# Optimization experiments

Measured on AMD Instinct MI355X. Metric: run time of the kernel, lower is better.

Reference implementation:

```python
import jax, jax.numpy as jnp
import numpy as np

N_SRC0, N_DST0 = 500000, 65536
N_DST1 = 8192
E0, E1 = 1048576, 131072
H = 4
SLOPE = 0.2


def gat_conv(h_src, h_dst, src, dst, Ws, Wd, al, ar, b, n_dst, act):
    # h_src: [Ns, Fin], Ws: [Fin, H*D]
    D = Ws.shape[1] // H
    fs = (h_src @ Ws).reshape(-1, H, D)          # [Ns,H,D]
    fd = (h_dst @ Wd).reshape(-1, H, D)          # [Nd,H,D]
    el = jnp.einsum('nhd,hd->nh', fs, al)        # [Ns,H]
    er = jnp.einsum('nhd,hd->nh', fd, ar)        # [Nd,H]
    e = jax.nn.leaky_relu(el[src] + er[dst], SLOPE)   # [E,H]
    m = jax.ops.segment_max(e, dst, num_segments=n_dst, indices_are_sorted=True)
    a = jnp.exp(e - m[dst])                      # [E,H]
    s = jax.ops.segment_sum(a, dst, num_segments=n_dst, indices_are_sorted=True)
    alpha = a / s[dst]                           # [E,H]
    msg = fs[src] * alpha[..., None]             # [E,H,D]
    out = jax.ops.segment_sum(msg, dst, num_segments=n_dst, indices_are_sorted=True) + b
    return act(out)                              # [Nd,H,D]


def setup_inputs() -> dict:
    key = jax.random.key(0)
    ks = jax.random.split(key, 16)
    D0, D1 = 64, 47
    inp = {
        'x': jax.random.normal(ks[0], (N_SRC0, 128), jnp.float32),
        'src0': jax.random.randint(ks[1], (E0,), 0, N_SRC0, jnp.int32),
        'dst0': jnp.sort(jax.random.randint(ks[2], (E0,), 0, N_DST0, jnp.int32)),
        'src1': jax.random.randint(ks[3], (E1,), 0, N_DST0, jnp.int32),
        'dst1': jnp.sort(jax.random.randint(ks[4], (E1,), 0, N_DST1, jnp.int32)),
        'Ws0': jax.random.normal(ks[5], (128, H * D0), jnp.float32) * 0.05,
        'Wd0': jax.random.normal(ks[6], (128, H * D0), jnp.float32) * 0.05,
        'al0': jax.random.normal(ks[7], (H, D0), jnp.float32) * 0.05,
        'ar0': jax.random.normal(ks[8], (H, D0), jnp.float32) * 0.05,
        'b0': jax.random.normal(ks[9], (H, D0), jnp.float32) * 0.05,
        'Ws1': jax.random.normal(ks[10], (H * D0, H * D1), jnp.float32) * 0.05,
        'Wd1': jax.random.normal(ks[11], (H * D0, H * D1), jnp.float32) * 0.05,
        'al1': jax.random.normal(ks[12], (H, D1), jnp.float32) * 0.05,
        'ar1': jax.random.normal(ks[13], (H, D1), jnp.float32) * 0.05,
        'b1': jax.random.normal(ks[14], (H, D1), jnp.float32) * 0.05,
    }
    return inp


def reference(x, src0, dst0, src1, dst1, Ws0, Wd0, al0, ar0, b0, Ws1, Wd1, al1, ar1, b1):
    # Layer 0: bipartite GATConv with ReLU, flatten heads
    h_dst = x[:N_DST0]
    h = gat_conv(x, h_dst, src0, dst0, Ws0, Wd0, al0, ar0, b0, N_DST0, jax.nn.relu)
    h = h.reshape(N_DST0, -1)                    # [N_DST0, H*D0]
    # Layer 1: no activation, mean over heads, log_softmax
    h_dst = h[:N_DST1]
    h = gat_conv(h, h_dst, src1, dst1, Ws1, Wd1, al1, ar1, b1, N_DST1, lambda z: z)
    h = h.mean(axis=1)                           # [N_DST1, D1]
    return jax.nn.log_softmax(h, axis=-1)
```

## Files before the change

kernel.cpp:

```cpp
#include <hip/hip_runtime.h>

typedef _Float16 half8  __attribute__((ext_vector_type(8)));
typedef _Float16 half4v __attribute__((ext_vector_type(4)));
typedef float    f32x4  __attribute__((ext_vector_type(4)));

#define GAT_SLOPE 0.2f
#define N_SRC0 500000
#define N_DST0 65536
#define N_DST1 8192
#define E0 1048576
#define E1 131072
#define H 4

__device__ __forceinline__ float leaky(float x) { return x >= 0.f ? x : GAT_SLOPE * x; }

__global__ void collapse_kernel(const float* __restrict__ W, const float* __restrict__ a,
                                float* __restrict__ out, int K, int D) {
  int i = blockIdx.x * 256 + threadIdx.x;
  if (i >= K * 4) return;
  int k = i >> 2, h = i & 3;
  int N = 4 * D;
  float s = 0.f;
  for (int d = 0; d < D; ++d) s += W[(size_t)k * N + h * D + d] * a[h * D + d];
  out[i] = s;
}

__global__ void transposeW_kernel(const float* __restrict__ W, _Float16* __restrict__ WT,
                                  int K, int N) {
  int i = blockIdx.x * 256 + threadIdx.x;
  if (i >= N * K) return;
  int nrow = i / K, k = i - nrow * K;
  WT[i] = (_Float16)W[(size_t)k * N + nrow];
}

__global__ void wstack_kernel(const float* __restrict__ W, _Float16* __restrict__ BTs) {
  int i = blockIdx.x * 256 + threadIdx.x;
  int n = i >> 10, kk = i & 1023;
  int h = kk >> 8, k = kk & 255;
  BTs[i] = (n < 47) ? (_Float16)(0.25f * W[(size_t)k * 188 + h * 47 + n]) : (_Float16)0.f;
}

__global__ void wlr_stack_kernel(const float* __restrict__ wl, const float* __restrict__ wr,
                                 _Float16* __restrict__ out, int K) {
  int i = blockIdx.x * 256 + threadIdx.x;
  if (i >= 16 * K) return;
  int n = i / K, k = i - n * K;
  float v = 0.f;
  if (n < 4) v = wl[k * 4 + n];
  else if (n < 8) v = wr[k * 4 + n - 4];
  out[i] = (_Float16)v;
}

__global__ void seg_starts_kernel(const int* __restrict__ dst, int E, int nseg,
                                  int* __restrict__ seg) {
  int i = blockIdx.x * 256 + threadIdx.x;
  if (i > E) return;
  int lo = (i == 0) ? 0 : dst[i - 1] + 1;
  int hi = (i == E) ? nseg : dst[i];
  for (int d = lo; d <= hi; ++d) seg[d] = i;
}

__global__ __launch_bounds__(256) void score_kernel(
    const int* __restrict__ src, const int* __restrict__ dst,
    const float* __restrict__ el, const float* __restrict__ er,
    float* __restrict__ alpha, int E) {
  int e = blockIdx.x * 256 + threadIdx.x;
  if (e >= E) return;
  int s = src[e], d = dst[e];
  float4 e4 = *(const float4*)(el + (size_t)s * 4);
  float4 r4 = *(const float4*)(er + (size_t)d * 4);
  float4 o;
  o.x = __expf(leaky(e4.x + r4.x));
  o.y = __expf(leaky(e4.y + r4.y));
  o.z = __expf(leaky(e4.z + r4.z));
  o.w = __expf(leaky(e4.w + r4.w));
  *(float4*)(alpha + (size_t)e * 4) = o;
}

__global__ __launch_bounds__(256) void cvt_elr_mfma_kernel(
    const float* __restrict__ x, const _Float16* __restrict__ WLR,
    _Float16* __restrict__ xh, float* __restrict__ el, float* __restrict__ er,
    int M, int n_dst) {
  __shared__ _Float16 As[128 * 128];
  const int t = threadIdx.x, lane = t & 63, wid = t >> 6;
  const int m0 = blockIdx.x * 128;
  for (int i = 0; i < 8; ++i) {
    int c = t + 256 * i;
    int row = c >> 4, j = c & 15;
    int gr = m0 + row;
    half8 va = {};
    if (gr < M) {
      float4 f0 = *(const float4*)(x + (size_t)gr * 128 + j * 8);
      float4 f1 = *(const float4*)(x + (size_t)gr * 128 + j * 8 + 4);
      va[0] = (_Float16)f0.x; va[1] = (_Float16)f0.y;
      va[2] = (_Float16)f0.z; va[3] = (_Float16)f0.w;
      va[4] = (_Float16)f1.x; va[5] = (_Float16)f1.y;
      va[6] = (_Float16)f1.z; va[7] = (_Float16)f1.w;
      *(half8*)(xh + (size_t)gr * 128 + j * 8) = va;
    }
    *(half8*)(&As[row * 128 + ((j ^ (row & 7)) << 3)]) = va;
  }
  half8 bf[4];
  for (int kc = 0; kc < 4; ++kc)
    bf[kc] = *(const half8*)(WLR + (lane & 15) * 128 + kc * 32 + (lane >> 4) * 8);
  __syncthreads();
  f32x4 acc[2] = {};
  for (int rt = 0; rt < 2; ++rt) {
    int row = (wid * 2 + rt) * 16 + (lane & 15);
    for (int kc = 0; kc < 4; ++kc) {
      int chunk = kc * 4 + (lane >> 4);
      half8 af = *(const half8*)(&As[row * 128 + ((chunk ^ (row & 7)) << 3)]);
      acc[rt] = __builtin_amdgcn_mfma_f32_16x16x32_f16(af, bf[kc], acc[rt], 0, 0, 0);
    }
  }
  int col = lane & 15, quad = lane >> 4;
  for (int rt = 0; rt < 2; ++rt)
    for (int r = 0; r < 4; ++r) {
      int row = m0 + (wid * 2 + rt) * 16 + quad * 4 + r;
      if (row < M) {
        if (col < 4) el[(size_t)row * 4 + col] = acc[rt][r];
        else if (col < 8 && row < n_dst) er[(size_t)row * 4 + col - 4] = acc[rt][r];
      }
    }
}

__global__ __launch_bounds__(256) void agg0w_kernel(
    const int* __restrict__ src, const int* __restrict__ seg,
    const float* __restrict__ alpha, const _Float16* __restrict__ xh,
    _Float16* __restrict__ axh) {
  const int lane = threadIdx.x & 63, w = threadIdx.x >> 6;
  const int n = blockIdx.x * 4 + w;
  int s0 = seg[n], s1 = seg[n + 1], len = s1 - s0;
  float a0 = 0.f, a1 = 0.f, a2 = 0.f, a3 = 0.f;
  float t0 = 0.f, t1 = 0.f, t2 = 0.f, t3 = 0.f;
  if (lane < len) {
    float4 v = *(const float4*)(alpha + (size_t)(s0 + lane) * 4);
    a0 = v.x; a1 = v.y; a2 = v.z; a3 = v.w;
    t0 = v.x; t1 = v.y; t2 = v.z; t3 = v.w;
  }
  for (int idx = 64 + lane; idx < len; idx += 64) {
    float4 v = *(const float4*)(alpha + (size_t)(s0 + idx) * 4);
    t0 += v.x; t1 += v.y; t2 += v.z; t3 += v.w;
  }
#pragma unroll
  for (int off = 32; off; off >>= 1) {
    t0 += __shfl_xor(t0, off); t1 += __shfl_xor(t1, off);
    t2 += __shfl_xor(t2, off); t3 += __shfl_xor(t3, off);
  }
  float sinv[4];
  sinv[0] = t0 > 0.f ? 1.f / t0 : 0.f;
  sinv[1] = t1 > 0.f ? 1.f / t1 : 0.f;
  sinv[2] = t2 > 0.f ? 1.f / t2 : 0.f;
  sinv[3] = t3 > 0.f ? 1.f / t3 : 0.f;
  const int g = lane >> 5, ci = lane & 31;
  float A[4][4] = {};
  int iters = (len + 1) >> 1;
  for (int k = 0; k < iters; ++k) {
    int idx = g + 2 * k;
    int sl = idx < 64 ? idx : 0;
    float ah0 = __shfl(a0, sl), ah1 = __shfl(a1, sl);
    float ah2 = __shfl(a2, sl), ah3 = __shfl(a3, sl);
    if (idx >= 64 && idx < len) {
      float4 v = *(const float4*)(alpha + (size_t)(s0 + idx) * 4);
      ah0 = v.x; ah1 = v.y; ah2 = v.z; ah3 = v.w;
    }
    if (idx < len) {
      int sidx = src[s0 + idx];
      half4v xv = *(const half4v*)(xh + (size_t)sidx * 128 + ci * 4);
#pragma unroll
      for (int c = 0; c < 4; ++c) {
        float xc = (float)xv[c];
        A[0][c] += ah0 * xc; A[1][c] += ah1 * xc;
        A[2][c] += ah2 * xc; A[3][c] += ah3 * xc;
      }
    }
  }
#pragma unroll
  for (int h = 0; h < 4; ++h)
#pragma unroll
    for (int c = 0; c < 4; ++c) A[h][c] += __shfl_xor(A[h][c], 32);
  if (g == 0) {
#pragma unroll
    for (int h = 0; h < 4; ++h) {
      half4v o;
#pragma unroll
      for (int c = 0; c < 4; ++c) o[c] = (_Float16)(A[h][c] * sinv[h]);
      *(half4v*)(axh + ((size_t)n * 4 + h) * 128 + ci * 4) = o;
    }
  }
}

__global__ __launch_bounds__(256) void agg1w_kernel(
    const int* __restrict__ src, const int* __restrict__ seg,
    const float* __restrict__ alpha, const _Float16* __restrict__ h0,
    _Float16* __restrict__ axh1) {
  const int lane = threadIdx.x & 63, w = threadIdx.x >> 6;
  const int n = blockIdx.x * 4 + w;
  int s0 = seg[n], s1 = seg[n + 1], len = s1 - s0;
  float a0 = 0.f, a1 = 0.f, a2 = 0.f, a3 = 0.f;
  float t0 = 0.f, t1 = 0.f, t2 = 0.f, t3 = 0.f;
  if (lane < len) {
    float4 v = *(const float4*)(alpha + (size_t)(s0 + lane) * 4);
    a0 = v.x; a1 = v.y; a2 = v.z; a3 = v.w;
    t0 = v.x; t1 = v.y; t2 = v.z; t3 = v.w;
  }
  for (int idx = 64 + lane; idx < len; idx += 64) {
    float4 v = *(const float4*)(alpha + (size_t)(s0 + idx) * 4);
    t0 += v.x; t1 += v.y; t2 += v.z; t3 += v.w;
  }
#pragma unroll
  for (int off = 32; off; off >>= 1) {
    t0 += __shfl_xor(t0, off); t1 += __shfl_xor(t1, off);
    t2 += __shfl_xor(t2, off); t3 += __shfl_xor(t3, off);
  }
  float sinv[4];
  sinv[0] = t0 > 0.f ? 1.f / t0 : 0.f;
  sinv[1] = t1 > 0.f ? 1.f / t1 : 0.f;
  sinv[2] = t2 > 0.f ? 1.f / t2 : 0.f;
  sinv[3] = t3 > 0.f ? 1.f / t3 : 0.f;
  const int g = lane >> 5, ci = lane & 31;
  float A[4][8] = {};
  int iters = (len + 1) >> 1;
  for (int k = 0; k < iters; ++k) {
    int idx = g + 2 * k;
    int sl = idx < 64 ? idx : 0;
    float ah0 = __shfl(a0, sl), ah1 = __shfl(a1, sl);
    float ah2 = __shfl(a2, sl), ah3 = __shfl(a3, sl);
    if (idx >= 64 && idx < len) {
      float4 v = *(const float4*)(alpha + (size_t)(s0 + idx) * 4);
      ah0 = v.x; ah1 = v.y; ah2 = v.z; ah3 = v.w;
    }
    if (idx < len) {
      int sidx = src[s0 + idx];
      half8 xv = *(const half8*)(h0 + (size_t)sidx * 256 + ci * 8);
#pragma unroll
      for (int c = 0; c < 8; ++c) {
        float xc = (float)xv[c];
        A[0][c] += ah0 * xc; A[1][c] += ah1 * xc;
        A[2][c] += ah2 * xc; A[3][c] += ah3 * xc;
      }
    }
  }
#pragma unroll
  for (int h = 0; h < 4; ++h)
#pragma unroll
    for (int c = 0; c < 8; ++c) A[h][c] += __shfl_xor(A[h][c], 32);
  if (g == 0) {
#pragma unroll
    for (int h = 0; h < 4; ++h) {
      half8 o;
#pragma unroll
      for (int c = 0; c < 8; ++c) o[c] = (_Float16)(A[h][c] * sinv[h]);
      *(half8*)(axh1 + ((size_t)n * 4 + h) * 256 + ci * 8) = o;
    }
  }
}

__global__ __launch_bounds__(256) void gemm_h0_kernel(
    const _Float16* __restrict__ axh, const _Float16* __restrict__ BT,
    const float* __restrict__ b, const float* __restrict__ wl1,
    const float* __restrict__ wr1, _Float16* __restrict__ h0,
    float* __restrict__ el1, float* __restrict__ er1) {
  __shared__ _Float16 As[128 * 128];
  __shared__ _Float16 Bs[64 * 128];
  const int t = threadIdx.x, lane = t & 63, wid = t >> 6;
  const int m0 = blockIdx.x * 128;
  const int cl = lane & 15, quad = lane >> 4;
  const int wm = wid * 32;
  f32x4 el1p[2][4] = {}, er1p[2][4] = {};
  for (int h = 0; h < 4; ++h) {
    for (int i = 0; i < 8; ++i) {
      int c = t + 256 * i, row = c >> 4, j = c & 15;
      int sw = ((j ^ (row & 7)) << 3);
      *(half8*)(&As[row * 128 + sw]) =
          *(const half8*)(axh + ((size_t)(m0 + row) * 4 + h) * 128 + j * 8);
    }
    for (int i = 0; i < 4; ++i) {
      int c = t + 256 * i, row = c >> 4, j = c & 15;
      int sw = ((j ^ (row & 7)) << 3);
      *(half8*)(&Bs[row * 128 + sw]) =
          *(const half8*)(BT + (size_t)(h * 64 + row) * 128 + j * 8);
    }
    __syncthreads();
    f32x4 acc[2][4] = {};
    for (int ks = 0; ks < 4; ++ks) {
      int kc = ks * 4 + quad;
      half8 af[2], bf[4];
      for (int i = 0; i < 2; ++i) {
        int ra = wm + 16 * i + cl;
        af[i] = *(const half8*)(&As[ra * 128 + ((kc ^ (ra & 7)) << 3)]);
      }
      for (int j2 = 0; j2 < 4; ++j2) {
        int rb = 16 * j2 + cl;
        bf[j2] = *(const half8*)(&Bs[rb * 128 + ((kc ^ (rb & 7)) << 3)]);
      }
      for (int i = 0; i < 2; ++i)
        for (int j2 = 0; j2 < 4; ++j2)
          acc[i][j2] = __builtin_amdgcn_mfma_f32_16x16x32_f16(af[i], bf[j2], acc[i][j2], 0, 0, 0);
    }
    __syncthreads();
    for (int j2 = 0; j2 < 4; ++j2) {
      int gcol = h * 64 + 16 * j2 + cl;
      float bias = b[gcol];
      f32x4 wlv = *(const f32x4*)(wl1 + (size_t)gcol * 4);
      f32x4 wrv = *(const f32x4*)(wr1 + (size_t)gcol * 4);
      for (int i = 0; i < 2; ++i) {
        int r0 = m0 + wm + 16 * i + quad * 4;
        for (int r = 0; r < 4; ++r) {
          float v = fmaxf(acc[i][j2][r] + bias, 0.f);
          h0[(size_t)(r0 + r) * 256 + gcol] = (_Float16)v;
          el1p[i][r] += wlv * v;
          er1p[i][r] += wrv * v;
        }
      }
    }
  }
#pragma unroll
  for (int off = 1; off < 16; off <<= 1)
#pragma unroll
    for (int i = 0; i < 2; ++i)
#pragma unroll
      for (int r = 0; r < 4; ++r)
#pragma unroll
        for (int c = 0; c < 4; ++c) {
          el1p[i][r][c] += __shfl_xor(el1p[i][r][c], off);
          er1p[i][r][c] += __shfl_xor(er1p[i][r][c], off);
        }
  if (cl == 0) {
    for (int i = 0; i < 2; ++i)
      for (int r = 0; r < 4; ++r) {
        int row = m0 + wm + 16 * i + quad * 4 + r;
        *(f32x4*)(el1 + (size_t)row * 4) = el1p[i][r];
        if (row < N_DST1) *(f32x4*)(er1 + (size_t)row * 4) = er1p[i][r];
      }
  }
}

__global__ __launch_bounds__(256) void gemm_out_kernel(
    const _Float16* __restrict__ axh1, const _Float16* __restrict__ BTs,
    const float* __restrict__ b1, float* __restrict__ out) {
  __shared__ _Float16 As[64 * 128];
  __shared__ _Float16 Bs[64 * 128];
  const int t = threadIdx.x, lane = t & 63, wid = t >> 6;
  const int m0 = blockIdx.x * 64;
  f32x4 acc[4] = {};
  for (int k0 = 0; k0 < 1024; k0 += 128) {
    for (int i = 0; i < 4; ++i) {
      int c = t + 256 * i, row = c >> 4, j = c & 15;
      int sw = ((j ^ (row & 7)) << 3);
      *(half8*)(&As[row * 128 + sw]) =
          *(const half8*)(axh1 + (size_t)(m0 + row) * 1024 + k0 + j * 8);
      *(half8*)(&Bs[row * 128 + sw]) =
          *(const half8*)(BTs + (size_t)row * 1024 + k0 + j * 8);
    }
    __syncthreads();
    const int wm = wid * 16;
    for (int ks = 0; ks < 4; ++ks) {
      int kc = ks * 4 + (lane >> 4);
      int ra = wm + (lane & 15);
      half8 af = *(const half8*)(&As[ra * 128 + ((kc ^ (ra & 7)) << 3)]);
      for (int j2 = 0; j2 < 4; ++j2) {
        int rb = 16 * j2 + (lane & 15);
        half8 bf = *(const half8*)(&Bs[rb * 128 + ((kc ^ (rb & 7)) << 3)]);
        acc[j2] = __builtin_amdgcn_mfma_f32_16x16x32_f16(af, bf, acc[j2], 0, 0, 0);
      }
    }
    __syncthreads();
  }
  int quad = lane >> 4, cl = lane & 15;
  float bm[3];
  for (int j2 = 0; j2 < 3; ++j2) {
    int col = 16 * j2 + cl;
    bm[j2] = (col < 47) ? 0.25f * (b1[col] + b1[col + 47] + b1[col + 94] + b1[col + 141]) : 0.f;
  }
  for (int r = 0; r < 4; ++r) {
    int row = m0 + wid * 16 + quad * 4 + r;
    float v[3];
    float mx = -1e30f;
    for (int j2 = 0; j2 < 3; ++j2) {
      int col = 16 * j2 + cl;
      v[j2] = acc[j2][r] + bm[j2];
      if (col < 47) mx = fmaxf(mx, v[j2]);
    }
    for (int off = 8; off; off >>= 1) mx = fmaxf(mx, __shfl_xor(mx, off));
    float s = 0.f;
    for (int j2 = 0; j2 < 3; ++j2) {
      int col = 16 * j2 + cl;
      if (col < 47) s += __expf(v[j2] - mx);
    }
    for (int off = 8; off; off >>= 1) s += __shfl_xor(s, off);
    float lse = mx + __logf(s);
    for (int j2 = 0; j2 < 3; ++j2) {
      int col = 16 * j2 + cl;
      if (col < 47) out[(size_t)row * 47 + col] = v[j2] - lse;
    }
  }
}

extern "C" void kernel_launch(void* const* d_in, const int* in_sizes, int n_in,
                              void* d_out, int out_size, void* d_ws, size_t ws_size,
                              hipStream_t stream) {
  const float* x   = (const float*)d_in[0];
  const int* src0  = (const int*)d_in[1];
  const int* dst0  = (const int*)d_in[2];
  const int* src1  = (const int*)d_in[3];
  const int* dst1  = (const int*)d_in[4];
  const float* Ws0 = (const float*)d_in[5];
  const float* Wd0 = (const float*)d_in[6];
  const float* al0 = (const float*)d_in[7];
  const float* ar0 = (const float*)d_in[8];
  const float* b0  = (const float*)d_in[9];
  const float* Ws1 = (const float*)d_in[10];
  const float* Wd1 = (const float*)d_in[11];
  const float* al1 = (const float*)d_in[12];
  const float* ar1 = (const float*)d_in[13];
  const float* b1  = (const float*)d_in[14];

  char* w = (char*)d_ws;
  auto alloc = [&](size_t bytes) {
    char* p = w;
    w += (bytes + 255) & ~(size_t)255;
    return p;
  };
  _Float16* xh   = (_Float16*)alloc((size_t)N_SRC0 * 128 * 2);
  _Float16* axh  = (_Float16*)alloc((size_t)N_DST0 * 512 * 2);
  _Float16* h0   = (_Float16*)alloc((size_t)N_DST0 * 256 * 2);
  _Float16* axh1 = (_Float16*)alloc((size_t)N_DST1 * 1024 * 2);
  float* el0     = (float*)alloc((size_t)N_SRC0 * 4 * 4);
  float* er0     = (float*)alloc((size_t)N_DST0 * 4 * 4);
  float* el1     = (float*)alloc((size_t)N_DST0 * 4 * 4);
  float* er1     = (float*)alloc((size_t)N_DST1 * 4 * 4);
  float* alpha0  = (float*)alloc((size_t)E0 * 4 * 4);
  float* alpha1  = (float*)alloc((size_t)E1 * 4 * 4);
  int* seg0      = (int*)alloc((size_t)(N_DST0 + 1) * 4);
  int* seg1      = (int*)alloc((size_t)(N_DST1 + 1) * 4);
  _Float16* BT0  = (_Float16*)alloc(256 * 128 * 2);
  _Float16* BTs  = (_Float16*)alloc(64 * 1024 * 2);
  _Float16* WLR0 = (_Float16*)alloc(16 * 128 * 2);
  float* wl0     = (float*)alloc(128 * 4 * 4);
  float* wr0     = (float*)alloc(128 * 4 * 4);
  float* wl1     = (float*)alloc(256 * 4 * 4);
  float* wr1     = (float*)alloc(256 * 4 * 4);

  collapse_kernel<<<2, 256, 0, stream>>>(Ws0, al0, wl0, 128, 64);
  collapse_kernel<<<2, 256, 0, stream>>>(Wd0, ar0, wr0, 128, 64);
  collapse_kernel<<<4, 256, 0, stream>>>(Ws1, al1, wl1, 256, 47);
  collapse_kernel<<<4, 256, 0, stream>>>(Wd1, ar1, wr1, 256, 47);
  wlr_stack_kernel<<<8, 256, 0, stream>>>(wl0, wr0, WLR0, 128);
  transposeW_kernel<<<128, 256, 0, stream>>>(Ws0, BT0, 128, 256);
  wstack_kernel<<<256, 256, 0, stream>>>(Ws1, BTs);
  seg_starts_kernel<<<(E0 + 1 + 255) / 256, 256, 0, stream>>>(dst0, E0, N_DST0, seg0);
  seg_starts_kernel<<<(E1 + 1 + 255) / 256, 256, 0, stream>>>(dst1, E1, N_DST1, seg1);
  cvt_elr_mfma_kernel<<<(N_SRC0 + 127) / 128, 256, 0, stream>>>(x, WLR0, xh, el0, er0,
                                                                N_SRC0, N_DST0);
  score_kernel<<<E0 / 256, 256, 0, stream>>>(src0, dst0, el0, er0, alpha0, E0);
  agg0w_kernel<<<N_DST0 / 4, 256, 0, stream>>>(src0, seg0, alpha0, xh, axh);
  gemm_h0_kernel<<<N_DST0 / 128, 256, 0, stream>>>(axh, BT0, b0, wl1, wr1, h0, el1, er1);
  score_kernel<<<E1 / 256, 256, 0, stream>>>(src1, dst1, el1, er1, alpha1, E1);
  agg1w_kernel<<<N_DST1 / 4, 256, 0, stream>>>(src1, seg1, alpha1, h0, axh1);
  gemm_out_kernel<<<N_DST1 / 64, 256, 0, stream>>>(axh1, BTs, b1, (float*)d_out);
}
```

Measured before the change: 641.7 us.

## Fuse edge scoring into aggregation kernels and merge prep kernels into one launch

Drops the separate score kernels that wrote per-edge exp scores to global memory. The aggregation kernels now compute leaky-relu and exp on the fly from el[src] and er[dst], and reuse the src index through a lane shuffle. The nine small setup kernels (weight collapse, transposes, segment starts) become one prep kernel. This removes the alpha buffers' write and read traffic and several launches, at the cost of extra exp work and el gathers inside the aggregation kernels.

Result: faster. 544.3 us (-15.2%).

```diff
diff --git a/kernel.cpp b/kernel.cpp
--- a/kernel.cpp
+++ b/kernel.cpp
@@ -14,68 +14,71 @@
 
 __device__ __forceinline__ float leaky(float x) { return x >= 0.f ? x : GAT_SLOPE * x; }
 
-__global__ void collapse_kernel(const float* __restrict__ W, const float* __restrict__ a,
-                                float* __restrict__ out, int K, int D) {
+__global__ __launch_bounds__(256) void prep_kernel(
+    const float* __restrict__ Ws0, const float* __restrict__ Wd0,
+    const float* __restrict__ al0, const float* __restrict__ ar0,
+    const float* __restrict__ Ws1, const float* __restrict__ Wd1,
+    const float* __restrict__ al1, const float* __restrict__ ar1,
+    const int* __restrict__ dst0, const int* __restrict__ dst1,
+    _Float16* __restrict__ BTs, _Float16* __restrict__ BT0,
+    _Float16* __restrict__ WLR0, float* __restrict__ wl1, float* __restrict__ wr1,
+    int* __restrict__ seg0, int* __restrict__ seg1) {
   int i = blockIdx.x * 256 + threadIdx.x;
-  if (i >= K * 4) return;
-  int k = i >> 2, h = i & 3;
-  int N = 4 * D;
-  float s = 0.f;
-  for (int d = 0; d < D; ++d) s += W[(size_t)k * N + h * D + d] * a[h * D + d];
-  out[i] = s;
-}
-
-__global__ void transposeW_kernel(const float* __restrict__ W, _Float16* __restrict__ WT,
-                                  int K, int N) {
-  int i = blockIdx.x * 256 + threadIdx.x;
-  if (i >= N * K) return;
-  int nrow = i / K, k = i - nrow * K;
-  WT[i] = (_Float16)W[(size_t)k * N + nrow];
-}
-
-__global__ void wstack_kernel(const float* __restrict__ W, _Float16* __restrict__ BTs) {
-  int i = blockIdx.x * 256 + threadIdx.x;
-  int n = i >> 10, kk = i & 1023;
-  int h = kk >> 8, k = kk & 255;
-  BTs[i] = (n < 47) ? (_Float16)(0.25f * W[(size_t)k * 188 + h * 47 + n]) : (_Float16)0.f;
-}
-
-__global__ void wlr_stack_kernel(const float* __restrict__ wl, const float* __restrict__ wr,
-                                 _Float16* __restrict__ out, int K) {
-  int i = blockIdx.x * 256 + threadIdx.x;
-  if (i >= 16 * K) return;
-  int n = i / K, k = i - n * K;
-  float v = 0.f;
-  if (n < 4) v = wl[k * 4 + n];
-  else if (n < 8) v = wr[k * 4 + n - 4];
-  out[i] = (_Float16)v;
-}
-
-__global__ void seg_starts_kernel(const int* __restrict__ dst, int E, int nseg,
-                                  int* __restrict__ seg) {
-  int i = blockIdx.x * 256 + threadIdx.x;
-  if (i > E) return;
-  int lo = (i == 0) ? 0 : dst[i - 1] + 1;
-  int hi = (i == E) ? nseg : dst[i];
-  for (int d = lo; d <= hi; ++d) seg[d] = i;
-}
-
-__global__ __launch_bounds__(256) void score_kernel(
-    const int* __restrict__ src, const int* __restrict__ dst,
-    const float* __restrict__ el, const float* __restrict__ er,
-    float* __restrict__ alpha, int E) {
-  int e = blockIdx.x * 256 + threadIdx.x;
-  if (e >= E) return;
-  int s = src[e], d = dst[e];
-  float4 e4 = *(const float4*)(el + (size_t)s * 4);
-  float4 r4 = *(const float4*)(er + (size_t)d * 4);
-  float4 o;
-  o.x = __expf(leaky(e4.x + r4.x));
-  o.y = __expf(leaky(e4.y + r4.y));
-  o.z = __expf(leaky(e4.z + r4.z));
-  o.w = __expf(leaky(e4.w + r4.w));
-  *(float4*)(alpha + (size_t)e * 4) = o;
-}
+  if (i < 65536) {
+    int n = i >> 10, kk = i & 1023, h = kk >> 8, k = kk & 255;
+    BTs[i] = (n < 47) ? (_Float16)(0.25f * Ws1[(size_t)k * 188 + h * 47 + n]) : (_Float16)0.f;
+    return;
+  }
+  i -= 65536;
+  if (i < 32768) {
+    int nrow = i >> 7, k = i & 127;
+    BT0[i] = (_Float16)Ws0[(size_t)k * 256 + nrow];
+    return;
+  }
+  i -= 32768;
+  if (i < 2048) {
+    int n = i >> 7, k = i & 127;
+    float v = 0.f;
+    if (n < 4) {
+      for (int d = 0; d < 64; ++d) v += Ws0[(size_t)k * 256 + n * 64 + d] * al0[n * 64 + d];
+    } else if (n < 8) {
+      int h = n - 4;
+      for (int d = 0; d < 64; ++d) v += Wd0[(size_t)k * 256 + h * 64 + d] * ar0[h * 64 + d];
+    }
+    WLR0[i] = (_Float16)v;
+    return;
+  }
+  i -= 2048;
+  if (i < 1024) {
+    int k = i >> 2, h = i & 3;
+    float v = 0.f;
+    for (int d = 0; d < 47; ++d) v += Ws1[(size_t)k * 188 + h * 47 + d] * al1[h * 47 + d];
+    wl1[i] = v;
+    return;
+  }
+  i -= 1024;
+  if (i < 1024) {
+    int k = i >> 2, h = i & 3;
+    float v = 0.f;
+    for (int d = 0; d < 47; ++d) v += Wd1[(size_t)k * 188 + h * 47 + d] * ar1[h * 47 + d];
+    wr1[i] = v;
+    return;
+  }
+  i -= 1024;
+  if (i <= E0) {
+    int lo = (i == 0) ? 0 : dst0[i - 1] + 1;
+    int hi = (i == E0) ? N_DST0 : dst0[i];
+    for (int d = lo; d <= hi; ++d) seg0[d] = i;
+    return;
+  }
+  i -= (E0 + 1);
+  if (i <= E1) {
+    int lo = (i == 0) ? 0 : dst1[i - 1] + 1;
+    int hi = (i == E1) ? N_DST1 : dst1[i];
+    for (int d = lo; d <= hi; ++d) seg1[d] = i;
+  }
+}
+#define PREP_TOTAL (65536 + 32768 + 2048 + 1024 + 1024 + (E0 + 1) + (E1 + 1))
 
 __global__ __launch_bounds__(256) void cvt_elr_mfma_kernel(
     const float* __restrict__ x, const _Float16* __restrict__ WLR,
@@ -124,34 +127,39 @@
     }
 }
 
-__global__ __launch_bounds__(256) void agg0w_kernel(
+__global__ __launch_bounds__(256) void agg0s_kernel(
     const int* __restrict__ src, const int* __restrict__ seg,
-    const float* __restrict__ alpha, const _Float16* __restrict__ xh,
-    _Float16* __restrict__ axh) {
+    const float* __restrict__ el, const float* __restrict__ er,
+    const _Float16* __restrict__ xh, _Float16* __restrict__ axh) {
   const int lane = threadIdx.x & 63, w = threadIdx.x >> 6;
   const int n = blockIdx.x * 4 + w;
-  int s0 = seg[n], s1 = seg[n + 1], len = s1 - s0;
+  int s0 = seg[n], len = seg[n + 1] - s0;
+  float4 erv = *(const float4*)(er + (size_t)n * 4);
   float a0 = 0.f, a1 = 0.f, a2 = 0.f, a3 = 0.f;
   float t0 = 0.f, t1 = 0.f, t2 = 0.f, t3 = 0.f;
+  int sreg = 0;
   if (lane < len) {
-    float4 v = *(const float4*)(alpha + (size_t)(s0 + lane) * 4);
-    a0 = v.x; a1 = v.y; a2 = v.z; a3 = v.w;
-    t0 = v.x; t1 = v.y; t2 = v.z; t3 = v.w;
+    sreg = src[s0 + lane];
+    float4 e4 = *(const float4*)(el + (size_t)sreg * 4);
+    a0 = __expf(leaky(e4.x + erv.x)); a1 = __expf(leaky(e4.y + erv.y));
+    a2 = __expf(leaky(e4.z + erv.z)); a3 = __expf(leaky(e4.w + erv.w));
+    t0 = a0; t1 = a1; t2 = a2; t3 = a3;
   }
   for (int idx = 64 + lane; idx < len; idx += 64) {
-    float4 v = *(const float4*)(alpha + (size_t)(s0 + idx) * 4);
-    t0 += v.x; t1 += v.y; t2 += v.z; t3 += v.w;
+    int s = src[s0 + idx];
+    float4 e4 = *(const float4*)(el + (size_t)s * 4);
+    t0 += __expf(leaky(e4.x + erv.x)); t1 += __expf(leaky(e4.y + erv.y));
+    t2 += __expf(leaky(e4.z + erv.z)); t3 += __expf(leaky(e4.w + erv.w));
   }
 #pragma unroll
   for (int off = 32; off; off >>= 1) {
     t0 += __shfl_xor(t0, off); t1 += __shfl_xor(t1, off);
     t2 += __shfl_xor(t2, off); t3 += __shfl_xor(t3, off);
   }
-  float sinv[4];
-  sinv[0] = t0 > 0.f ? 1.f / t0 : 0.f;
-  sinv[1] = t1 > 0.f ? 1.f / t1 : 0.f;
-  sinv[2] = t2 > 0.f ? 1.f / t2 : 0.f;
-  sinv[3] = t3 > 0.f ? 1.f / t3 : 0.f;
+  float si0 = t0 > 0.f ? 1.f / t0 : 0.f;
+  float si1 = t1 > 0.f ? 1.f / t1 : 0.f;
+  float si2 = t2 > 0.f ? 1.f / t2 : 0.f;
+  float si3 = t3 > 0.f ? 1.f / t3 : 0.f;
   const int g = lane >> 5, ci = lane & 31;
   float A[4][4] = {};
   int iters = (len + 1) >> 1;
@@ -160,12 +168,14 @@
     int sl = idx < 64 ? idx : 0;
     float ah0 = __shfl(a0, sl), ah1 = __shfl(a1, sl);
     float ah2 = __shfl(a2, sl), ah3 = __shfl(a3, sl);
+    int sidx = __shfl(sreg, sl);
     if (idx >= 64 && idx < len) {
-      float4 v = *(const float4*)(alpha + (size_t)(s0 + idx) * 4);
-      ah0 = v.x; ah1 = v.y; ah2 = v.z; ah3 = v.w;
+      sidx = src[s0 + idx];
+      float4 e4 = *(const float4*)(el + (size_t)sidx * 4);
+      ah0 = __expf(leaky(e4.x + erv.x)); ah1 = __expf(leaky(e4.y + erv.y));
+      ah2 = __expf(leaky(e4.z + erv.z)); ah3 = __expf(leaky(e4.w + erv.w));
     }
     if (idx < len) {
-      int sidx = src[s0 + idx];
       half4v xv = *(const half4v*)(xh + (size_t)sidx * 128 + ci * 4);
 #pragma unroll
       for (int c = 0; c < 4; ++c) {
@@ -180,44 +190,50 @@
 #pragma unroll
     for (int c = 0; c < 4; ++c) A[h][c] += __shfl_xor(A[h][c], 32);
   if (g == 0) {
+    float si[4] = {si0, si1, si2, si3};
 #pragma unroll
     for (int h = 0; h < 4; ++h) {
       half4v o;
 #pragma unroll
-      for (int c = 0; c < 4; ++c) o[c] = (_Float16)(A[h][c] * sinv[h]);
+      for (int c = 0; c < 4; ++c) o[c] = (_Float16)(A[h][c] * si[h]);
       *(half4v*)(axh + ((size_t)n * 4 + h) * 128 + ci * 4) = o;
     }
   }
 }
 
-__global__ __launch_bounds__(256) void agg1w_kernel(
+__global__ __launch_bounds__(256) void agg1s_kernel(
     const int* __restrict__ src, const int* __restrict__ seg,
-    const float* __restrict__ alpha, const _Float16* __restrict__ h0,
-    _Float16* __restrict__ axh1) {
+    const float* __restrict__ el, const float* __restrict__ er,
+    const _Float16* __restrict__ h0, _Float16* __restrict__ axh1) {
   const int lane = threadIdx.x & 63, w = threadIdx.x >> 6;
   const int n = blockIdx.x * 4 + w;
-  int s0 = seg[n], s1 = seg[n + 1], len = s1 - s0;
+  int s0 = seg[n], len = seg[n + 1] - s0;
+  float4 erv = *(const float4*)(er + (size_t)n * 4);
   float a0 = 0.f, a1 = 0.f, a2 = 0.f, a3 = 0.f;
   float t0 = 0.f, t1 = 0.f, t2 = 0.f, t3 = 0.f;
+  int sreg = 0;
   if (lane < len) {
-    float4 v = *(const float4*)(alpha + (size_t)(s0 + lane) * 4);
-    a0 = v.x; a1 = v.y; a2 = v.z; a3 = v.w;
-    t0 = v.x; t1 = v.y; t2 = v.z; t3 = v.w;
+    sreg = src[s0 + lane];
+    float4 e4 = *(const float4*)(el + (size_t)sreg * 4);
+    a0 = __expf(leaky(e4.x + erv.x)); a1 = __expf(leaky(e4.y + erv.y));
+    a2 = __expf(leaky(e4.z + erv.z)); a3 = __expf(leaky(e4.w + erv.w));
+    t0 = a0; t1 = a1; t2 = a2; t3 = a3;
   }
   for (int idx = 64 + lane; idx < len; idx += 64) {
-    float4 v = *(const float4*)(alpha + (size_t)(s0 + idx) * 4);
-    t0 += v.x; t1 += v.y; t2 += v.z; t3 += v.w;
+    int s = src[s0 + idx];
+    float4 e4 = *(const float4*)(el + (size_t)s * 4);
+    t0 += __expf(leaky(e4.x + erv.x)); t1 += __expf(leaky(e4.y + erv.y));
+    t2 += __expf(leaky(e4.z + erv.z)); t3 += __expf(leaky(e4.w + erv.w));
   }
 #pragma unroll
   for (int off = 32; off; off >>= 1) {
     t0 += __shfl_xor(t0, off); t1 += __shfl_xor(t1, off);
     t2 += __shfl_xor(t2, off); t3 += __shfl_xor(t3, off);
   }
-  float sinv[4];
-  sinv[0] = t0 > 0.f ? 1.f / t0 : 0.f;
-  sinv[1] = t1 > 0.f ? 1.f / t1 : 0.f;
-  sinv[2] = t2 > 0.f ? 1.f / t2 : 0.f;
-  sinv[3] = t3 > 0.f ? 1.f / t3 : 0.f;
+  float si0 = t0 > 0.f ? 1.f / t0 : 0.f;
+  float si1 = t1 > 0.f ? 1.f / t1 : 0.f;
+  float si2 = t2 > 0.f ? 1.f / t2 : 0.f;
+  float si3 = t3 > 0.f ? 1.f / t3 : 0.f;
   const int g = lane >> 5, ci = lane & 31;
   float A[4][8] = {};
   int iters = (len + 1) >> 1;
@@ -226,12 +242,14 @@
     int sl = idx < 64 ? idx : 0;
     float ah0 = __shfl(a0, sl), ah1 = __shfl(a1, sl);
     float ah2 = __shfl(a2, sl), ah3 = __shfl(a3, sl);
+    int sidx = __shfl(sreg, sl);
     if (idx >= 64 && idx < len) {
-      float4 v = *(const float4*)(alpha + (size_t)(s0 + idx) * 4);
-      ah0 = v.x; ah1 = v.y; ah2 = v.z; ah3 = v.w;
+      sidx = src[s0 + idx];
+      float4 e4 = *(const float4*)(el + (size_t)sidx * 4);
+      ah0 = __expf(leaky(e4.x + erv.x)); ah1 = __expf(leaky(e4.y + erv.y));
+      ah2 = __expf(leaky(e4.z + erv.z)); ah3 = __expf(leaky(e4.w + erv.w));
     }
     if (idx < len) {
-      int sidx = src[s0 + idx];
       half8 xv = *(const half8*)(h0 + (size_t)sidx * 256 + ci * 8);
 #pragma unroll
       for (int c = 0; c < 8; ++c) {
@@ -246,11 +264,12 @@
 #pragma unroll
     for (int c = 0; c < 8; ++c) A[h][c] += __shfl_xor(A[h][c], 32);
   if (g == 0) {
+    float si[4] = {si0, si1, si2, si3};
 #pragma unroll
     for (int h = 0; h < 4; ++h) {
       half8 o;
 #pragma unroll
-      for (int c = 0; c < 8; ++c) o[c] = (_Float16)(A[h][c] * sinv[h]);
+      for (int c = 0; c < 8; ++c) o[c] = (_Float16)(A[h][c] * si[h]);
       *(half8*)(axh1 + ((size_t)n * 4 + h) * 256 + ci * 8) = o;
     }
   }
@@ -430,33 +449,21 @@
   float* er0     = (float*)alloc((size_t)N_DST0 * 4 * 4);
   float* el1     = (float*)alloc((size_t)N_DST0 * 4 * 4);
   float* er1     = (float*)alloc((size_t)N_DST1 * 4 * 4);
-  float* alpha0  = (float*)alloc((size_t)E0 * 4 * 4);
-  float* alpha1  = (float*)alloc((size_t)E1 * 4 * 4);
   int* seg0      = (int*)alloc((size_t)(N_DST0 + 1) * 4);
   int* seg1      = (int*)alloc((size_t)(N_DST1 + 1) * 4);
   _Float16* BT0  = (_Float16*)alloc(256 * 128 * 2);
   _Float16* BTs  = (_Float16*)alloc(64 * 1024 * 2);
   _Float16* WLR0 = (_Float16*)alloc(16 * 128 * 2);
-  float* wl0     = (float*)alloc(128 * 4 * 4);
-  float* wr0     = (float*)alloc(128 * 4 * 4);
   float* wl1     = (float*)alloc(256 * 4 * 4);
   float* wr1     = (float*)alloc(256 * 4 * 4);
 
-  collapse_kernel<<<2, 256, 0, stream>>>(Ws0, al0, wl0, 128, 64);
-  collapse_kernel<<<2, 256, 0, stream>>>(Wd0, ar0, wr0, 128, 64);
-  collapse_kernel<<<4, 256, 0, stream>>>(Ws1, al1, wl1, 256, 47);
-  collapse_kernel<<<4, 256, 0, stream>>>(Wd1, ar1, wr1, 256, 47);
-  wlr_stack_kernel<<<8, 256, 0, stream>>>(wl0, wr0, WLR0, 128);
-  transposeW_kernel<<<128, 256, 0, stream>>>(Ws0, BT0, 128, 256);
-  wstack_kernel<<<256, 256, 0, stream>>>(Ws1, BTs);
-  seg_starts_kernel<<<(E0 + 1 + 255) / 256, 256, 0, stream>>>(dst0, E0, N_DST0, seg0);
-  seg_starts_kernel<<<(E1 + 1 + 255) / 256, 256, 0, stream>>>(dst1, E1, N_DST1, seg1);
+  prep_kernel<<<(PREP_TOTAL + 255) / 256, 256, 0, stream>>>(
+      Ws0, Wd0, al0, ar0, Ws1, Wd1, al1, ar1, dst0, dst1,
+      BTs, BT0, WLR0, wl1, wr1, seg0, seg1);
   cvt_elr_mfma_kernel<<<(N_SRC0 + 127) / 128, 256, 0, stream>>>(x, WLR0, xh, el0, er0,
                                                                 N_SRC0, N_DST0);
-  score_kernel<<<E0 / 256, 256, 0, stream>>>(src0, dst0, el0, er0, alpha0, E0);
-  agg0w_kernel<<<N_DST0 / 4, 256, 0, stream>>>(src0, seg0, alpha0, xh, axh);
+  agg0s_kernel<<<N_DST0 / 4, 256, 0, stream>>>(src0, seg0, el0, er0, xh, axh);
   gemm_h0_kernel<<<N_DST0 / 128, 256, 0, stream>>>(axh, BT0, b0, wl1, wr1, h0, el1, er1);
-  score_kernel<<<E1 / 256, 256, 0, stream>>>(src1, dst1, el1, er1, alpha1, E1);
-  agg1w_kernel<<<N_DST1 / 4, 256, 0, stream>>>(src1, seg1, alpha1, h0, axh1);
+  agg1s_kernel<<<N_DST1 / 4, 256, 0, stream>>>(src1, seg1, el1, er1, h0, axh1);
   gemm_out_kernel<<<N_DST1 / 64, 256, 0, stream>>>(axh1, BTs, b1, (float*)d_out);
 }
```
